# Performance work log

Hardware: AMD Instinct MI355X
Metric: run time of the kernel (lower is better)

The kernel has to match this reference:

```python
import jax, jax.numpy as jnp
import numpy as np

H = 64  # hidden_dim


def _gru_cell(x, h, W_ih, W_hh, b_ih, b_hh):
    # PyTorch GRU gate order: reset (r), update (z), new (n)
    gx = x @ W_ih.T + b_ih            # [B, 3H]
    gh = h @ W_hh.T + b_hh            # [B, 3H]
    xr, xz, xn = jnp.split(gx, 3, axis=-1)
    hr, hz, hn = jnp.split(gh, 3, axis=-1)
    r = jax.nn.sigmoid(xr + hr)
    z = jax.nn.sigmoid(xz + hz)
    n = jnp.tanh(xn + r * hn)
    return (1.0 - z) * n + z * h


def setup_inputs() -> dict:
    key = jax.random.key(0)
    ks = jax.random.split(key, 11)
    B, T, F_in, A = 1024, 512, 128, 18
    s = 0.05
    return {
        "state": jax.random.normal(ks[0], (B, T, F_in), dtype=jnp.float32),
        "W_ih_l0": jax.random.normal(ks[1], (3 * H, F_in), dtype=jnp.float32) * s,
        "W_hh_l0": jax.random.normal(ks[2], (3 * H, H), dtype=jnp.float32) * s,
        "b_ih_l0": jax.random.normal(ks[3], (3 * H,), dtype=jnp.float32) * s,
        "b_hh_l0": jax.random.normal(ks[4], (3 * H,), dtype=jnp.float32) * s,
        "W_ih_l1": jax.random.normal(ks[5], (3 * H, H), dtype=jnp.float32) * s,
        "W_hh_l1": jax.random.normal(ks[6], (3 * H, H), dtype=jnp.float32) * s,
        "b_ih_l1": jax.random.normal(ks[7], (3 * H,), dtype=jnp.float32) * s,
        "b_hh_l1": jax.random.normal(ks[8], (3 * H,), dtype=jnp.float32) * s,
        "fc3_w": jax.random.normal(ks[9], (A, H), dtype=jnp.float32) * s,
        "fc3_b": jax.random.normal(ks[10], (A,), dtype=jnp.float32) * s,
    }


def reference(state, W_ih_l0, W_hh_l0, b_ih_l0, b_hh_l0,
              W_ih_l1, W_hh_l1, b_ih_l1, b_hh_l1, fc3_w, fc3_b):
    B = state.shape[0]
    h0 = jnp.zeros((B, H), dtype=state.dtype)
    h1 = jnp.zeros((B, H), dtype=state.dtype)
    xs = jnp.swapaxes(state, 0, 1)  # [T, B, F]

    def step(carry, x_t):
        h0, h1 = carry
        h0 = _gru_cell(x_t, h0, W_ih_l0, W_hh_l0, b_ih_l0, b_hh_l0)
        h1 = _gru_cell(h0, h1, W_ih_l1, W_hh_l1, b_ih_l1, b_hh_l1)
        return (h0, h1), None

    (_, h1_last), _ = jax.lax.scan(step, (h0, h1), xs)
    # out[:, -1] of the top GRU layer == final h1; then relu -> linear
    actions = jax.nn.relu(h1_last) @ fc3_w.T + fc3_b
    return actions
```

## Files before the change

kernel.cpp:

```cpp
#include <hip/hip_runtime.h>


#define Tn 512
#define Fn 128
#define Hn 64
#define An 18
#define HS 72

#define S_RZ (-1.4426950408889634f)
#define S_N  (-2.8853900817779268f)

typedef _Float16 half8 __attribute__((ext_vector_type(8)));
typedef _Float16 half4 __attribute__((ext_vector_type(4)));
typedef float f32x4 __attribute__((ext_vector_type(4)));

#define MFMA(w, d, c) __builtin_amdgcn_mfma_f32_16x16x32_f16((w), (d), (c), 0, 0, 0)

static __device__ __forceinline__ float sigm_s(float x) {
    return __builtin_amdgcn_rcpf(1.0f + __builtin_amdgcn_exp2f(x));
}
static __device__ __forceinline__ float tanh_s(float x) {
    return 2.0f * __builtin_amdgcn_rcpf(1.0f + __builtin_amdgcn_exp2f(x)) - 1.0f;
}

__global__ __launch_bounds__(768) void gru_fused(
    const float* __restrict__ state,
    const float* __restrict__ Wih0, const float* __restrict__ Whh0,
    const float* __restrict__ bih0, const float* __restrict__ bhh0,
    const float* __restrict__ Wih1, const float* __restrict__ Whh1,
    const float* __restrict__ bih1, const float* __restrict__ bhh1,
    const float* __restrict__ fcw, const float* __restrict__ fcb,
    float* __restrict__ out)
{
    const int tid  = threadIdx.x;
    const int wv12 = tid >> 6;
    const int lane = tid & 63, c = lane & 15, q = lane >> 4;
    const int wv   = wv12 & 3;
    const int r0   = blockIdx.x * 16;
    const int gc   = wv * 16 + c;
    const int cb   = wv * 16 + q * 4;
    const int role = (wv12 < 4) ? 0 : (wv12 < 8 ? 1 : 2);

    __shared__ __align__(16) float    gxring[2][4][3][64][4];
    __shared__ __align__(16) _Float16 h0buf[2][16 * HS];
    __shared__ __align__(16) _Float16 h1buf[2][16 * HS];
    __shared__ float fbuf[16 * 64];

    for (int i = tid; i < 2 * 16 * HS; i += 768) {
        (&h0buf[0][0])[i] = (_Float16)0.0f;
        (&h1buf[0][0])[i] = (_Float16)0.0f;
    }

    half8 W[12];
    f32x4 bias0, bias1, bias2, bias3;
    f32x4 xf32[8];
    f32x4 hreg = {0.f, 0.f, 0.f, 0.f};
    const float* srow = state + (size_t)(r0 + c) * (Tn * Fn);

    if (role == 0) {
#pragma unroll
        for (int gsel = 0; gsel < 3; ++gsel) {
            const float s = (gsel < 2) ? S_RZ : S_N;
            const int g = gsel * 64 + gc;
#pragma unroll
            for (int ks = 0; ks < 4; ++ks) {
                const float* p = Wih0 + g * Fn + ks * 32 + q * 8;
#pragma unroll
                for (int j = 0; j < 8; ++j) W[gsel * 4 + ks][j] = (_Float16)(s * p[j]);
            }
        }
        {
            const f32x4 bi0 = *(const f32x4*)&bih0[cb]       , bh0 = *(const f32x4*)&bhh0[cb];
            const f32x4 bi1 = *(const f32x4*)&bih0[64 + cb]  , bh1 = *(const f32x4*)&bhh0[64 + cb];
            const f32x4 bi2 = *(const f32x4*)&bih0[128 + cb];
            bias0 = (bi0 + bh0) * S_RZ;
            bias1 = (bi1 + bh1) * S_RZ;
            bias2 = bi2 * S_N;
        }
#pragma unroll
        for (int ks = 0; ks < 4; ++ks) {
            xf32[2 * ks]     = *(const f32x4*)(srow + ks * 32 + q * 8);
            xf32[2 * ks + 1] = *(const f32x4*)(srow + ks * 32 + q * 8 + 4);
        }
        half8 xf[4];
#pragma unroll
        for (int ks = 0; ks < 4; ++ks)
#pragma unroll
            for (int i = 0; i < 4; ++i) {
                xf[ks][i]     = (_Float16)xf32[2 * ks][i];
                xf[ks][4 + i] = (_Float16)xf32[2 * ks + 1][i];
            }
        f32x4 a0 = bias0, a1 = bias1, a2 = bias2;
#pragma unroll
        for (int ks = 0; ks < 4; ++ks) {
            a0 = MFMA(W[ks],     xf[ks], a0);
            a1 = MFMA(W[4 + ks], xf[ks], a1);
            a2 = MFMA(W[8 + ks], xf[ks], a2);
        }
        *(f32x4*)&gxring[0][wv][0][lane][0] = a0;
        *(f32x4*)&gxring[0][wv][1][lane][0] = a1;
        *(f32x4*)&gxring[0][wv][2][lane][0] = a2;
#pragma unroll
        for (int ks = 0; ks < 4; ++ks) {
            xf32[2 * ks]     = *(const f32x4*)(srow + Fn + ks * 32 + q * 8);
            xf32[2 * ks + 1] = *(const f32x4*)(srow + Fn + ks * 32 + q * 8 + 4);
        }
    } else if (role == 1) {
#pragma unroll
        for (int gsel = 0; gsel < 3; ++gsel) {
            const float s = (gsel < 2) ? S_RZ : S_N;
            const int g = gsel * 64 + gc;
#pragma unroll
            for (int ks = 0; ks < 2; ++ks) {
                const float* p = Whh0 + g * Hn + ks * 32 + q * 8;
#pragma unroll
                for (int j = 0; j < 8; ++j) W[gsel * 2 + ks][j] = (_Float16)(s * p[j]);
            }
        }
        bias3 = (*(const f32x4*)&bhh0[128 + cb]) * S_N;
    } else {
#pragma unroll
        for (int gsel = 0; gsel < 3; ++gsel) {
            const float s = (gsel < 2) ? S_RZ : S_N;
            const int g = gsel * 64 + gc;
#pragma unroll
            for (int ks = 0; ks < 2; ++ks) {
                const float* pa = Wih1 + g * Hn + ks * 32 + q * 8;
                const float* pb = Whh1 + g * Hn + ks * 32 + q * 8;
#pragma unroll
                for (int j = 0; j < 8; ++j) {
                    W[gsel * 2 + ks][j]     = (_Float16)(s * pa[j]);
                    W[6 + gsel * 2 + ks][j] = (_Float16)(s * pb[j]);
                }
            }
        }
        const f32x4 bi0 = *(const f32x4*)&bih1[cb]      , bh0 = *(const f32x4*)&bhh1[cb];
        const f32x4 bi1 = *(const f32x4*)&bih1[64 + cb] , bh1 = *(const f32x4*)&bhh1[64 + cb];
        bias0 = (bi0 + bh0) * S_RZ;
        bias1 = (bi1 + bh1) * S_RZ;
        bias2 = (*(const f32x4*)&bih1[128 + cb]) * S_N;
        bias3 = (*(const f32x4*)&bhh1[128 + cb]) * S_N;
    }

    const int ardr = c * HS + q * 8;
    const int wofs = c * HS + cb;

    for (int t = 0; t <= Tn; ++t) {
        __syncthreads();
        const int pr = (t & 1) ^ 1, pw = t & 1;
        if (role == 0) {
            if (t < Tn - 1) {
                half8 xf[4];
#pragma unroll
                for (int ks = 0; ks < 4; ++ks)
#pragma unroll
                    for (int i = 0; i < 4; ++i) {
                        xf[ks][i]     = (_Float16)xf32[2 * ks][i];
                        xf[ks][4 + i] = (_Float16)xf32[2 * ks + 1][i];
                    }
                const int tnx = (t + 2 < Tn) ? (t + 2) : (Tn - 1);
#pragma unroll
                for (int ks = 0; ks < 4; ++ks) {
                    xf32[2 * ks]     = *(const f32x4*)(srow + (size_t)tnx * Fn + ks * 32 + q * 8);
                    xf32[2 * ks + 1] = *(const f32x4*)(srow + (size_t)tnx * Fn + ks * 32 + q * 8 + 4);
                }
                f32x4 a0 = bias0, a1 = bias1, a2 = bias2;
#pragma unroll
                for (int ks = 0; ks < 4; ++ks) {
                    a0 = MFMA(W[ks],     xf[ks], a0);
                    a1 = MFMA(W[4 + ks], xf[ks], a1);
                    a2 = MFMA(W[8 + ks], xf[ks], a2);
                }
                const int slot = (t + 1) & 1;
                *(f32x4*)&gxring[slot][wv][0][lane][0] = a0;
                *(f32x4*)&gxring[slot][wv][1][lane][0] = a1;
                *(f32x4*)&gxring[slot][wv][2][lane][0] = a2;
            }
        } else if (role == 1) {
            if (t < Tn) {
                f32x4 accr  = *(const f32x4*)&gxring[t & 1][wv][0][lane][0];
                f32x4 accz  = *(const f32x4*)&gxring[t & 1][wv][1][lane][0];
                f32x4 accxn = *(const f32x4*)&gxring[t & 1][wv][2][lane][0];
                const half8 hf0 = *(const half8*)&h0buf[pr][ardr];
                const half8 hf1 = *(const half8*)&h0buf[pr][ardr + 32];
                accr = MFMA(W[0], hf0, accr);
                accr = MFMA(W[1], hf1, accr);
                accz = MFMA(W[2], hf0, accz);
                accz = MFMA(W[3], hf1, accz);
                f32x4 acchn = MFMA(W[4], hf0, bias3);
                acchn = MFMA(W[5], hf1, acchn);
                half4 hw;
#pragma unroll
                for (int i = 0; i < 4; ++i) {
                    const float rg = sigm_s(accr[i]);
                    const float zg = sigm_s(accz[i]);
                    const float ng = tanh_s(accxn[i] + rg * acchn[i]);
                    hreg[i] = ng + zg * (hreg[i] - ng);
                    hw[i] = (_Float16)hreg[i];
                }
                *(half4*)&h0buf[pw][wofs] = hw;
            }
        } else {
            if (t >= 1) {
                const half8 xf0 = *(const half8*)&h0buf[pr][ardr];
                const half8 xf1 = *(const half8*)&h0buf[pr][ardr + 32];
                const half8 hf0 = *(const half8*)&h1buf[pw][ardr];
                const half8 hf1 = *(const half8*)&h1buf[pw][ardr + 32];
                f32x4 accr = MFMA(W[0], xf0, bias0);
                accr = MFMA(W[1], xf1, accr);
                f32x4 accz = MFMA(W[2], xf0, bias1);
                accz = MFMA(W[3], xf1, accz);
                f32x4 accxn = MFMA(W[4], xf0, bias2);
                accxn = MFMA(W[5], xf1, accxn);
                accr = MFMA(W[6], hf0, accr);
                accr = MFMA(W[7], hf1, accr);
                accz = MFMA(W[8], hf0, accz);
                accz = MFMA(W[9], hf1, accz);
                f32x4 acchn = MFMA(W[10], hf0, bias3);
                acchn = MFMA(W[11], hf1, acchn);
                half4 hw;
#pragma unroll
                for (int i = 0; i < 4; ++i) {
                    const float rg = sigm_s(accr[i]);
                    const float zg = sigm_s(accz[i]);
                    const float ng = tanh_s(accxn[i] + rg * acchn[i]);
                    hreg[i] = ng + zg * (hreg[i] - ng);
                    hw[i] = (_Float16)hreg[i];
                }
                *(half4*)&h1buf[pr][wofs] = hw;
            }
        }
    }

    if (role == 2) {
        f32x4 fv;
#pragma unroll
        for (int i = 0; i < 4; ++i) fv[i] = fmaxf(hreg[i], 0.0f);
        *(f32x4*)&fbuf[c * 64 + cb] = fv;
    }
    __syncthreads();
    for (int idx = tid; idx < 16 * An; idx += 768) {
        const int row = idx / An, a = idx - row * An;
        float acc = fcb[a];
#pragma unroll 16
        for (int k = 0; k < Hn; ++k) acc += fbuf[row * 64 + k] * fcw[a * Hn + k];
        out[(size_t)(r0 + row) * An + a] = acc;
    }
}

extern "C" void kernel_launch(void* const* d_in, const int* in_sizes, int n_in,
                              void* d_out, int out_size, void* d_ws, size_t ws_size,
                              hipStream_t stream) {
    const float* state = (const float*)d_in[0];
    const float* Wih0  = (const float*)d_in[1];
    const float* Whh0  = (const float*)d_in[2];
    const float* bih0  = (const float*)d_in[3];
    const float* bhh0  = (const float*)d_in[4];
    const float* Wih1  = (const float*)d_in[5];
    const float* Whh1  = (const float*)d_in[6];
    const float* bih1  = (const float*)d_in[7];
    const float* bhh1  = (const float*)d_in[8];
    const float* fcw   = (const float*)d_in[9];
    const float* fcb   = (const float*)d_in[10];
    float* out = (float*)d_out;

    gru_fused<<<64, 768, 0, stream>>>(state, Wih0, Whh0, bih0, bhh0,
                                      Wih1, Whh1, bih1, bhh1, fcw, fcb, out);
}
```

Before: 741.7 us.

## Deepen GRU wavefront pipeline and hoist input projections off recurrent critical path

The gx ring grows from two to four slots, and the layer-0 input projection now runs two steps ahead. The recurrent wave preloads the next step's gx values into registers after writing h, so the LDS read leaves the critical path. Layer 1 splits its input projection (from h0) into a separate stage computed one step early, so each step's critical chain holds only the six recurrent MFMAs plus gates. This adds one more loop iteration of pipeline latency and extra registers in exchange for shorter per-step dependency chains.

```diff
diff --git a/kernel.cpp b/kernel.cpp
--- a/kernel.cpp
+++ b/kernel.cpp
@@ -41,7 +41,7 @@
     const int cb   = wv * 16 + q * 4;
     const int role = (wv12 < 4) ? 0 : (wv12 < 8 ? 1 : 2);
 
-    __shared__ __align__(16) float    gxring[2][4][3][64][4];
+    __shared__ __align__(16) float    gxring[4][4][3][64][4];
     __shared__ __align__(16) _Float16 h0buf[2][16 * HS];
     __shared__ __align__(16) _Float16 h1buf[2][16 * HS];
     __shared__ float fbuf[16 * 64];
@@ -55,7 +55,13 @@
     f32x4 bias0, bias1, bias2, bias3;
     f32x4 xf32[8];
     f32x4 hreg = {0.f, 0.f, 0.f, 0.f};
+    const f32x4 z4 = {0.f, 0.f, 0.f, 0.f};
+    f32x4 gxp0 = z4, gxp1 = z4, gxp2 = z4;
+    f32x4 gxa0 = z4, gxa1 = z4, gxa2 = z4;
     const float* srow = state + (size_t)(r0 + c) * (Tn * Fn);
+
+    const int ardr = c * HS + q * 8;
+    const int wofs = c * HS + cb;
 
     if (role == 0) {
 #pragma unroll
@@ -70,40 +76,42 @@
             }
         }
         {
-            const f32x4 bi0 = *(const f32x4*)&bih0[cb]       , bh0 = *(const f32x4*)&bhh0[cb];
-            const f32x4 bi1 = *(const f32x4*)&bih0[64 + cb]  , bh1 = *(const f32x4*)&bhh0[64 + cb];
-            const f32x4 bi2 = *(const f32x4*)&bih0[128 + cb];
+            const f32x4 bi0 = *(const f32x4*)&bih0[cb]      , bh0 = *(const f32x4*)&bhh0[cb];
+            const f32x4 bi1 = *(const f32x4*)&bih0[64 + cb] , bh1 = *(const f32x4*)&bhh0[64 + cb];
             bias0 = (bi0 + bh0) * S_RZ;
             bias1 = (bi1 + bh1) * S_RZ;
-            bias2 = bi2 * S_N;
+            bias2 = (*(const f32x4*)&bih0[128 + cb]) * S_N;
+        }
+#pragma unroll
+        for (int tt = 0; tt < 2; ++tt) {
+#pragma unroll
+            for (int ks = 0; ks < 4; ++ks) {
+                xf32[2 * ks]     = *(const f32x4*)(srow + tt * Fn + ks * 32 + q * 8);
+                xf32[2 * ks + 1] = *(const f32x4*)(srow + tt * Fn + ks * 32 + q * 8 + 4);
+            }
+            half8 xf[4];
+#pragma unroll
+            for (int ks = 0; ks < 4; ++ks)
+#pragma unroll
+                for (int i = 0; i < 4; ++i) {
+                    xf[ks][i]     = (_Float16)xf32[2 * ks][i];
+                    xf[ks][4 + i] = (_Float16)xf32[2 * ks + 1][i];
+                }
+            f32x4 a0 = bias0, a1 = bias1, a2 = bias2;
+#pragma unroll
+            for (int ks = 0; ks < 4; ++ks) {
+                a0 = MFMA(W[ks],     xf[ks], a0);
+                a1 = MFMA(W[4 + ks], xf[ks], a1);
+                a2 = MFMA(W[8 + ks], xf[ks], a2);
+            }
+            *(f32x4*)&gxring[tt][wv][0][lane][0] = a0;
+            *(f32x4*)&gxring[tt][wv][1][lane][0] = a1;
+            *(f32x4*)&gxring[tt][wv][2][lane][0] = a2;
         }
 #pragma unroll
         for (int ks = 0; ks < 4; ++ks) {
-            xf32[2 * ks]     = *(const f32x4*)(srow + ks * 32 + q * 8);
-            xf32[2 * ks + 1] = *(const f32x4*)(srow + ks * 32 + q * 8 + 4);
-        }
-        half8 xf[4];
-#pragma unroll
-        for (int ks = 0; ks < 4; ++ks)
-#pragma unroll
-            for (int i = 0; i < 4; ++i) {
-                xf[ks][i]     = (_Float16)xf32[2 * ks][i];
-                xf[ks][4 + i] = (_Float16)xf32[2 * ks + 1][i];
-            }
-        f32x4 a0 = bias0, a1 = bias1, a2 = bias2;
-#pragma unroll
-        for (int ks = 0; ks < 4; ++ks) {
-            a0 = MFMA(W[ks],     xf[ks], a0);
-            a1 = MFMA(W[4 + ks], xf[ks], a1);
-            a2 = MFMA(W[8 + ks], xf[ks], a2);
-        }
-        *(f32x4*)&gxring[0][wv][0][lane][0] = a0;
-        *(f32x4*)&gxring[0][wv][1][lane][0] = a1;
-        *(f32x4*)&gxring[0][wv][2][lane][0] = a2;
-#pragma unroll
-        for (int ks = 0; ks < 4; ++ks) {
-            xf32[2 * ks]     = *(const f32x4*)(srow + Fn + ks * 32 + q * 8);
-            xf32[2 * ks + 1] = *(const f32x4*)(srow + Fn + ks * 32 + q * 8 + 4);
+            xf32[2 * ks]     = *(const f32x4*)(srow + 2 * Fn + ks * 32 + q * 8);
+            xf32[2 * ks + 1] = *(const f32x4*)(srow + 2 * Fn + ks * 32 + q * 8 + 4);
         }
     } else if (role == 1) {
 #pragma unroll
@@ -142,14 +150,17 @@
         bias3 = (*(const f32x4*)&bhh1[128 + cb]) * S_N;
     }
 
-    const int ardr = c * HS + q * 8;
-    const int wofs = c * HS + cb;
-
-    for (int t = 0; t <= Tn; ++t) {
+    __syncthreads();
+    if (role == 1) {
+        gxp0 = *(const f32x4*)&gxring[0][wv][0][lane][0];
+        gxp1 = *(const f32x4*)&gxring[0][wv][1][lane][0];
+        gxp2 = *(const f32x4*)&gxring[0][wv][2][lane][0];
+    }
+
+    for (int t = 0; t <= Tn + 1; ++t) {
         __syncthreads();
-        const int pr = (t & 1) ^ 1, pw = t & 1;
         if (role == 0) {
-            if (t < Tn - 1) {
+            if (t <= Tn - 3) {
                 half8 xf[4];
 #pragma unroll
                 for (int ks = 0; ks < 4; ++ks)
@@ -158,11 +169,13 @@
                         xf[ks][i]     = (_Float16)xf32[2 * ks][i];
                         xf[ks][4 + i] = (_Float16)xf32[2 * ks + 1][i];
                     }
-                const int tnx = (t + 2 < Tn) ? (t + 2) : (Tn - 1);
-#pragma unroll
-                for (int ks = 0; ks < 4; ++ks) {
-                    xf32[2 * ks]     = *(const f32x4*)(srow + (size_t)tnx * Fn + ks * 32 + q * 8);
-                    xf32[2 * ks + 1] = *(const f32x4*)(srow + (size_t)tnx * Fn + ks * 32 + q * 8 + 4);
+                if (t <= Tn - 4) {
+                    const int tnx = t + 3;
+#pragma unroll
+                    for (int ks = 0; ks < 4; ++ks) {
+                        xf32[2 * ks]     = *(const f32x4*)(srow + (size_t)tnx * Fn + ks * 32 + q * 8);
+                        xf32[2 * ks + 1] = *(const f32x4*)(srow + (size_t)tnx * Fn + ks * 32 + q * 8 + 4);
+                    }
                 }
                 f32x4 a0 = bias0, a1 = bias1, a2 = bias2;
 #pragma unroll
@@ -171,63 +184,64 @@
                     a1 = MFMA(W[4 + ks], xf[ks], a1);
                     a2 = MFMA(W[8 + ks], xf[ks], a2);
                 }
-                const int slot = (t + 1) & 1;
+                const int slot = (t + 2) & 3;
                 *(f32x4*)&gxring[slot][wv][0][lane][0] = a0;
                 *(f32x4*)&gxring[slot][wv][1][lane][0] = a1;
                 *(f32x4*)&gxring[slot][wv][2][lane][0] = a2;
             }
         } else if (role == 1) {
             if (t < Tn) {
-                f32x4 accr  = *(const f32x4*)&gxring[t & 1][wv][0][lane][0];
-                f32x4 accz  = *(const f32x4*)&gxring[t & 1][wv][1][lane][0];
-                f32x4 accxn = *(const f32x4*)&gxring[t & 1][wv][2][lane][0];
+                const int pr = (t + 1) & 1, pw = t & 1;
                 const half8 hf0 = *(const half8*)&h0buf[pr][ardr];
                 const half8 hf1 = *(const half8*)&h0buf[pr][ardr + 32];
-                accr = MFMA(W[0], hf0, accr);
-                accr = MFMA(W[1], hf1, accr);
-                accz = MFMA(W[2], hf0, accz);
-                accz = MFMA(W[3], hf1, accz);
-                f32x4 acchn = MFMA(W[4], hf0, bias3);
-                acchn = MFMA(W[5], hf1, acchn);
+                f32x4 hr = MFMA(W[0], hf0, z4);    hr = MFMA(W[1], hf1, hr);
+                f32x4 hz = MFMA(W[2], hf0, z4);    hz = MFMA(W[3], hf1, hz);
+                f32x4 hn = MFMA(W[4], hf0, bias3); hn = MFMA(W[5], hf1, hn);
+                const f32x4 accr = gxp0 + hr;
+                const f32x4 accz = gxp1 + hz;
                 half4 hw;
 #pragma unroll
                 for (int i = 0; i < 4; ++i) {
                     const float rg = sigm_s(accr[i]);
                     const float zg = sigm_s(accz[i]);
-                    const float ng = tanh_s(accxn[i] + rg * acchn[i]);
+                    const float ng = tanh_s(gxp2[i] + rg * hn[i]);
                     hreg[i] = ng + zg * (hreg[i] - ng);
                     hw[i] = (_Float16)hreg[i];
                 }
                 *(half4*)&h0buf[pw][wofs] = hw;
+                if (t + 1 < Tn) {
+                    const int ns = (t + 1) & 3;
+                    gxp0 = *(const f32x4*)&gxring[ns][wv][0][lane][0];
+                    gxp1 = *(const f32x4*)&gxring[ns][wv][1][lane][0];
+                    gxp2 = *(const f32x4*)&gxring[ns][wv][2][lane][0];
+                }
             }
         } else {
-            if (t >= 1) {
-                const half8 xf0 = *(const half8*)&h0buf[pr][ardr];
-                const half8 xf1 = *(const half8*)&h0buf[pr][ardr + 32];
-                const half8 hf0 = *(const half8*)&h1buf[pw][ardr];
-                const half8 hf1 = *(const half8*)&h1buf[pw][ardr + 32];
-                f32x4 accr = MFMA(W[0], xf0, bias0);
-                accr = MFMA(W[1], xf1, accr);
-                f32x4 accz = MFMA(W[2], xf0, bias1);
-                accz = MFMA(W[3], xf1, accz);
-                f32x4 accxn = MFMA(W[4], xf0, bias2);
-                accxn = MFMA(W[5], xf1, accxn);
-                accr = MFMA(W[6], hf0, accr);
-                accr = MFMA(W[7], hf1, accr);
-                accz = MFMA(W[8], hf0, accz);
-                accz = MFMA(W[9], hf1, accz);
-                f32x4 acchn = MFMA(W[10], hf0, bias3);
-                acchn = MFMA(W[11], hf1, acchn);
+            if (t >= 2) {
+                const half8 hf0 = *(const half8*)&h1buf[(t + 1) & 1][ardr];
+                const half8 hf1 = *(const half8*)&h1buf[(t + 1) & 1][ardr + 32];
+                f32x4 hr = MFMA(W[6], hf0, z4);     hr = MFMA(W[7], hf1, hr);
+                f32x4 hz = MFMA(W[8], hf0, z4);     hz = MFMA(W[9], hf1, hz);
+                f32x4 hn = MFMA(W[10], hf0, bias3); hn = MFMA(W[11], hf1, hn);
+                const f32x4 accr = gxa0 + hr;
+                const f32x4 accz = gxa1 + hz;
                 half4 hw;
 #pragma unroll
                 for (int i = 0; i < 4; ++i) {
                     const float rg = sigm_s(accr[i]);
                     const float zg = sigm_s(accz[i]);
-                    const float ng = tanh_s(accxn[i] + rg * acchn[i]);
+                    const float ng = tanh_s(gxa2[i] + rg * hn[i]);
                     hreg[i] = ng + zg * (hreg[i] - ng);
                     hw[i] = (_Float16)hreg[i];
                 }
-                *(half4*)&h1buf[pr][wofs] = hw;
+                *(half4*)&h1buf[t & 1][wofs] = hw;
+            }
+            if (t >= 1 && t <= Tn) {
+                const half8 xf0 = *(const half8*)&h0buf[(t + 1) & 1][ardr];
+                const half8 xf1 = *(const half8*)&h0buf[(t + 1) & 1][ardr + 32];
+                gxa0 = MFMA(W[0], xf0, bias0); gxa0 = MFMA(W[1], xf1, gxa0);
+                gxa1 = MFMA(W[2], xf0, bias1); gxa1 = MFMA(W[3], xf1, gxa1);
+                gxa2 = MFMA(W[4], xf0, bias2); gxa2 = MFMA(W[5], xf1, gxa2);
             }
         }
     }
```

New measurement: 1.072 ms. 1.45x slower.
